# Kernel optimization log

Hardware: AMD Instinct MI355X
Metric: run time of the kernel (lower is better)

The kernel has to match this reference:

```python
import jax, jax.numpy as jnp
import numpy as np

N_NODES = 65536
IN_DIM = 512
OUT_DIM = 512
N_EDGES = 524288
BN_EPS = 1e-5
NORM_EPS = 1e-6


def setup_inputs() -> dict:
    key = jax.random.key(0)
    k1, k2, k3, k4 = jax.random.split(key, 4)
    features = jax.random.normal(k1, (N_NODES, IN_DIM), dtype=jnp.float32)
    edge_index = jax.random.randint(k2, (2, N_EDGES), 0, N_NODES, dtype=jnp.int64)
    # torch Linear weight layout: [out_features, in_features] with in = 2*IN_DIM
    W = jax.random.normal(k3, (OUT_DIM, 2 * IN_DIM), dtype=jnp.float32) * (1.0 / np.sqrt(2 * IN_DIM))
    b = jax.random.normal(k4, (OUT_DIM,), dtype=jnp.float32) * 0.01
    gamma = jnp.ones((OUT_DIM,), dtype=jnp.float32)
    beta = jnp.zeros((OUT_DIM,), dtype=jnp.float32)
    running_mean = jnp.zeros((OUT_DIM,), dtype=jnp.float32)
    running_var = jnp.ones((OUT_DIM,), dtype=jnp.float32)
    return {
        "features": features,
        "edge_index": edge_index,
        "W": W,
        "b": b,
        "gamma": gamma,
        "beta": beta,
        "running_mean": running_mean,
        "running_var": running_var,
    }


def reference(features, edge_index, W, b, gamma, beta, running_mean, running_var):
    sources = edge_index[0]
    targets = edge_index[1]
    # scatter-sum of neighbor (target) features into source rows  [N, D]
    aggregated = jax.ops.segment_sum(features[targets], sources, num_segments=N_NODES)
    out = jnp.concatenate([features, aggregated], axis=1)  # [N, 2D]
    out = out @ W.T + b  # [N, OUT_DIM]
    out = jax.nn.relu(out)
    # BatchNorm1d (eval mode, running stats)
    out = (out - running_mean) * jax.lax.rsqrt(running_var + BN_EPS) * gamma + beta
    # dropout is identity in inference
    out = out / (jnp.linalg.norm(out, axis=1, keepdims=True) + NORM_EPS)
    return out
```

## Files before the change

### kernel.cpp

```cpp
#include <hip/hip_runtime.h>
#include <hip/hip_bf16.h>

#define N_NODES 65536
#define DIM 512
#define N_EDGES 524288
#define BN_EPS 1e-5f
#define NORM_EPS 1e-6f

typedef __attribute__((ext_vector_type(8))) short short8;
typedef __attribute__((ext_vector_type(4))) float f32x4;

static __device__ __forceinline__ unsigned f2bf(float f) {
    union { float f; unsigned u; } c; c.f = f;
    unsigned u = c.u;
    return (u + 0x7fffu + ((u >> 16) & 1u)) >> 16;
}
static __device__ __forceinline__ float bf16lo(unsigned u) {
    union { unsigned u; float f; } c; c.u = u << 16; return c.f;
}
static __device__ __forceinline__ float bf16hi(unsigned u) {
    union { unsigned u; float f; } c; c.u = u & 0xffff0000u; return c.f;
}
static __device__ __forceinline__ uint4 pack8(float4 a, float4 b) {
    uint4 o;
    o.x = f2bf(a.x) | (f2bf(a.y) << 16);
    o.y = f2bf(a.z) | (f2bf(a.w) << 16);
    o.z = f2bf(b.x) | (f2bf(b.y) << 16);
    o.w = f2bf(b.z) | (f2bf(b.w) << 16);
    return o;
}

__global__ void convert_kernel(const float* __restrict__ src,
                               unsigned short* __restrict__ dst, int n8) {
    int i = blockIdx.x * blockDim.x + threadIdx.x;
    if (i < n8) {
        const float4* s = (const float4*)src + i * 2;
        float4 f0 = s[0], f1 = s[1];
        ((uint4*)dst)[i] = pack8(f0, f1);
    }
}

__global__ void hist_kernel(const int* __restrict__ src, int* __restrict__ counts) {
    int e = blockIdx.x * blockDim.x + threadIdx.x;
    if (e < N_EDGES) atomicAdd(&counts[src[e]], 1);
}

__global__ void scan_partial(const int* __restrict__ counts, int* __restrict__ partials) {
    __shared__ int ws[4];
    int t = threadIdx.x;
    int v = counts[blockIdx.x * 256 + t];
#pragma unroll
    for (int d = 1; d < 64; d <<= 1) v += __shfl_xor(v, d);
    if ((t & 63) == 0) ws[t >> 6] = v;
    __syncthreads();
    if (t == 0) partials[blockIdx.x] = ws[0] + ws[1] + ws[2] + ws[3];
}

__global__ void scan_base(int* __restrict__ partials) {
    __shared__ int lds[256];
    int t = threadIdx.x;
    int v = partials[t];
    lds[t] = v;
    __syncthreads();
    for (int d = 1; d < 256; d <<= 1) {
        int mine = lds[t];
        int add = (t >= d) ? lds[t - d] : 0;
        __syncthreads();
        lds[t] = mine + add;
        __syncthreads();
    }
    partials[t] = lds[t] - v;
}

__global__ void scan_final(const int* __restrict__ counts,
                           const int* __restrict__ partials,
                           int* __restrict__ offsets, int* __restrict__ cursor) {
    __shared__ int lds[256];
    int t = threadIdx.x, b = blockIdx.x;
    int v = counts[b * 256 + t];
    lds[t] = v;
    __syncthreads();
    for (int d = 1; d < 256; d <<= 1) {
        int mine = lds[t];
        int add = (t >= d) ? lds[t - d] : 0;
        __syncthreads();
        lds[t] = mine + add;
        __syncthreads();
    }
    int excl = lds[t] - v + partials[b];
    offsets[b * 256 + t] = excl;
    cursor[b * 256 + t] = excl;
    if (b == 255 && t == 255) offsets[N_NODES] = excl + v;
}

__global__ void scatter_kernel(const int* __restrict__ src, const int* __restrict__ tgt,
                               int* __restrict__ cursor, int* __restrict__ sortedT) {
    int e = blockIdx.x * blockDim.x + threadIdx.x;
    if (e < N_EDGES) {
        int s = src[e];
        int pos = atomicAdd(&cursor[s], 1);
        sortedT[pos] = tgt[e];
    }
}

static __device__ __forceinline__ void acc8(float* a, uint4 v) {
    a[0] += bf16lo(v.x); a[1] += bf16hi(v.x);
    a[2] += bf16lo(v.y); a[3] += bf16hi(v.y);
    a[4] += bf16lo(v.z); a[5] += bf16hi(v.z);
    a[6] += bf16lo(v.w); a[7] += bf16hi(v.w);
}

__global__ void aggregate_kernel(const unsigned short* __restrict__ Xb,
                                 const int* __restrict__ offsets,
                                 const int* __restrict__ sortedT,
                                 unsigned short* __restrict__ agg) {
    int wave = (blockIdx.x * blockDim.x + threadIdx.x) >> 6;
    int lane = threadIdx.x & 63;
    if (wave >= N_NODES) return;
    int beg = offsets[wave], end = offsets[wave + 1];
    float a[8] = {0.f, 0.f, 0.f, 0.f, 0.f, 0.f, 0.f, 0.f};
    float b[8] = {0.f, 0.f, 0.f, 0.f, 0.f, 0.f, 0.f, 0.f};
    const uint4* F = (const uint4*)Xb;
    int i = beg;
    for (; i + 4 <= end; i += 4) {
        int t0 = sortedT[i], t1 = sortedT[i + 1], t2 = sortedT[i + 2], t3 = sortedT[i + 3];
        uint4 v0 = F[t0 * 64 + lane];
        uint4 v1 = F[t1 * 64 + lane];
        uint4 v2 = F[t2 * 64 + lane];
        uint4 v3 = F[t3 * 64 + lane];
        acc8(a, v0); acc8(b, v1); acc8(a, v2); acc8(b, v3);
    }
    if (i + 2 <= end) {
        int t0 = sortedT[i], t1 = sortedT[i + 1];
        uint4 v0 = F[t0 * 64 + lane];
        uint4 v1 = F[t1 * 64 + lane];
        acc8(a, v0); acc8(b, v1);
        i += 2;
    }
    if (i < end) {
        int t0 = sortedT[i];
        uint4 v0 = F[t0 * 64 + lane];
        acc8(a, v0);
    }
#pragma unroll
    for (int k = 0; k < 8; ++k) a[k] += b[k];
    uint4 o;
    o.x = f2bf(a[0]) | (f2bf(a[1]) << 16);
    o.y = f2bf(a[2]) | (f2bf(a[3]) << 16);
    o.z = f2bf(a[4]) | (f2bf(a[5]) << 16);
    o.w = f2bf(a[6]) | (f2bf(a[7]) << 16);
    ((uint4*)agg)[wave * 64 + lane] = o;
}

__global__ __launch_bounds__(512, 2) void fused_gemm_norm_kernel(
        const unsigned short* __restrict__ Xb,
        const unsigned short* __restrict__ agg,
        const unsigned short* __restrict__ Wb,
        const float* __restrict__ bias,
        const float* __restrict__ gamma,
        const float* __restrict__ beta,
        const float* __restrict__ rmean,
        const float* __restrict__ rvar,
        float* __restrict__ out) {
    __shared__ uint4 Abuf[2][512];
    __shared__ uint4 Bbuf[2][4096];
    float (*ssm)[8] = reinterpret_cast<float (*)[8]>(&Abuf[0][0]);

    const int t = threadIdx.x;
    const int m0 = blockIdx.x * 64;
    const int w = t >> 6, L = t & 63;
    const int ml = L & 15, quad = L >> 4;
    const int wn = w * 64;

    auto stage = [&](int buf, int kt) {
        const unsigned short* Asrc = (kt < 8) ? (Xb + kt * 64) : (agg + (kt - 8) * 64);
        {
            int r = t >> 3, pp = t & 7;
            int p = pp ^ (r & 7);
            const unsigned short* ga = Asrc + (m0 + r) * 512 + p * 8;
            char* la = (char*)&Abuf[buf][t & 448];
            __builtin_amdgcn_global_load_lds(
                (const __attribute__((address_space(1))) unsigned int*)ga,
                (__attribute__((address_space(3))) unsigned int*)la, 16, 0, 0);
        }
#pragma unroll
        for (int j = 0; j < 8; ++j) {
            int c = j * 64 + L;
            int rl = c >> 3, pp = c & 7;
            int p = pp ^ (rl & 7);
            const unsigned short* gb = Wb + (wn + rl) * 1024 + kt * 64 + p * 8;
            char* lb = (char*)&Bbuf[buf][w * 512 + j * 64];
            __builtin_amdgcn_global_load_lds(
                (const __attribute__((address_space(1))) unsigned int*)gb,
                (__attribute__((address_space(3))) unsigned int*)lb, 16, 0, 0);
        }
    };

    f32x4 acc[4][4];
#pragma unroll
    for (int mi = 0; mi < 4; ++mi)
#pragma unroll
        for (int ni = 0; ni < 4; ++ni)
            acc[mi][ni] = (f32x4){0.f, 0.f, 0.f, 0.f};

    stage(0, 0);
    __syncthreads();

    int cur = 0;
    for (int kt = 0; kt < 16; ++kt) {
        if (kt < 15) stage(cur ^ 1, kt + 1);
#pragma unroll
        for (int kc = 0; kc < 2; ++kc) {
            int g = kc * 4 + quad;
            short8 a[4], b[4];
#pragma unroll
            for (int mi = 0; mi < 4; ++mi) {
                int ra = mi * 16 + ml;
                a[mi] = *(const short8*)&Abuf[cur][ra * 8 + (g ^ (ra & 7))];
                int rl = mi * 16 + ml;
                b[mi] = *(const short8*)&Bbuf[cur][w * 512 + rl * 8 + (g ^ (rl & 7))];
            }
#pragma unroll
            for (int mi = 0; mi < 4; ++mi)
#pragma unroll
                for (int ni = 0; ni < 4; ++ni)
                    acc[mi][ni] = __builtin_amdgcn_mfma_f32_16x16x32_bf16(
                        a[mi], b[ni], acc[mi][ni], 0, 0, 0);
        }
        __syncthreads();
        cur ^= 1;
    }

    float bi[4], sc[4], sh[4];
#pragma unroll
    for (int ni = 0; ni < 4; ++ni) {
        int col = wn + ni * 16 + ml;
        bi[ni] = bias[col];
        sc[ni] = gamma[col] * __frsqrt_rn(rvar[col] + BN_EPS);
        sh[ni] = beta[col] - rmean[col] * sc[ni];
    }
    float ss[4][4];
#pragma unroll
    for (int mi = 0; mi < 4; ++mi)
#pragma unroll
        for (int r = 0; r < 4; ++r)
            ss[mi][r] = 0.f;
#pragma unroll
    for (int mi = 0; mi < 4; ++mi)
#pragma unroll
        for (int ni = 0; ni < 4; ++ni)
#pragma unroll
            for (int r = 0; r < 4; ++r) {
                float v = fmaxf(acc[mi][ni][r] + bi[ni], 0.f) * sc[ni] + sh[ni];
                acc[mi][ni][r] = v;
                ss[mi][r] += v * v;
            }
#pragma unroll
    for (int mi = 0; mi < 4; ++mi)
#pragma unroll
        for (int r = 0; r < 4; ++r) {
#pragma unroll
            for (int d = 1; d < 16; d <<= 1)
                ss[mi][r] += __shfl_xor(ss[mi][r], d);
        }
    if (ml == 0) {
#pragma unroll
        for (int mi = 0; mi < 4; ++mi)
#pragma unroll
            for (int r = 0; r < 4; ++r)
                ssm[mi * 16 + quad * 4 + r][w] = ss[mi][r];
    }
    __syncthreads();
#pragma unroll
    for (int mi = 0; mi < 4; ++mi)
#pragma unroll
        for (int r = 0; r < 4; ++r) {
            int rl = mi * 16 + quad * 4 + r;
            const float4* sp = (const float4*)ssm[rl];
            float4 s0 = sp[0], s1 = sp[1];
            float tot = s0.x + s0.y + s0.z + s0.w + s1.x + s1.y + s1.z + s1.w;
            float inv = 1.f / (sqrtf(tot) + NORM_EPS);
            int m = m0 + rl;
#pragma unroll
            for (int ni = 0; ni < 4; ++ni)
                out[m * 512 + wn + ni * 16 + ml] = acc[mi][ni][r] * inv;
        }
}

extern "C" void kernel_launch(void* const* d_in, const int* in_sizes, int n_in,
                              void* d_out, int out_size, void* d_ws, size_t ws_size,
                              hipStream_t stream) {
    const float* features = (const float*)d_in[0];
    const int* edges      = (const int*)d_in[1];
    const float* W        = (const float*)d_in[2];
    const float* bias     = (const float*)d_in[3];
    const float* gamma    = (const float*)d_in[4];
    const float* beta     = (const float*)d_in[5];
    const float* rmean    = (const float*)d_in[6];
    const float* rvar     = (const float*)d_in[7];
    float* out = (float*)d_out;

    char* ws = (char*)d_ws;
    int* counts   = (int*)(ws);
    int* offsets  = (int*)(ws + 0x100000);
    int* cursor   = (int*)(ws + 0x200000);
    int* partials = (int*)(ws + 0x280000);
    int* sortedT  = (int*)(ws + 0x300000);
    unsigned short* Wb  = (unsigned short*)(ws + 0x500000);
    unsigned short* Xb  = (unsigned short*)(ws + 0x600000);
    unsigned short* agg = (unsigned short*)(ws + 0x4600000);

    const int* src = edges;
    const int* tgt = edges + N_EDGES;

    hipMemsetAsync(counts, 0, N_NODES * sizeof(int), stream);
    hist_kernel<<<N_EDGES / 256, 256, 0, stream>>>(src, counts);
    scan_partial<<<256, 256, 0, stream>>>(counts, partials);
    scan_base<<<1, 256, 0, stream>>>(partials);
    scan_final<<<256, 256, 0, stream>>>(counts, partials, offsets, cursor);
    scatter_kernel<<<N_EDGES / 256, 256, 0, stream>>>(src, tgt, cursor, sortedT);
    convert_kernel<<<(N_NODES * DIM / 8) / 256, 256, 0, stream>>>(features, Xb, N_NODES * DIM / 8);
    convert_kernel<<<(DIM * 2 * DIM / 8) / 256, 256, 0, stream>>>(W, Wb, DIM * 2 * DIM / 8);
    aggregate_kernel<<<N_NODES / 4, 256, 0, stream>>>(Xb, offsets, sortedT, agg);
    fused_gemm_norm_kernel<<<N_NODES / 64, 512, 0, stream>>>(
        Xb, agg, Wb, bias, gamma, beta, rmean, rvar, out);
}
```

Measured before the change: 495.0 us.

## Double GEMM row tile to 128 with 16 waves and finer-grained waitcnt sync

The fused GEMM+norm kernel now runs 1024-thread blocks covering 128 rows, arranged as a 2x8 wave grid, so each staged W tile is shared by twice as many rows and W reload traffic is halved. The per-wave B staging becomes a cooperative block-wide load, and the full __syncthreads pairs are replaced by explicit vmcnt/lgkmcnt waits plus raw s_barrier so the next stage's loads can stay in flight. The cost is larger LDS use per block and a launch_bounds of (1024,4) that may tighten register limits and cause spills. Fewer, larger blocks also reduce the number of blocks per CU.

```diff
diff --git a/kernel.cpp b/kernel.cpp
--- a/kernel.cpp
+++ b/kernel.cpp
@@ -152,7 +152,7 @@
     ((uint4*)agg)[wave * 64 + lane] = o;
 }
 
-__global__ __launch_bounds__(512, 2) void fused_gemm_norm_kernel(
+__global__ __launch_bounds__(1024, 4) void fused_gemm_norm_kernel(
         const unsigned short* __restrict__ Xb,
         const unsigned short* __restrict__ agg,
         const unsigned short* __restrict__ Wb,
@@ -162,15 +162,16 @@
         const float* __restrict__ rmean,
         const float* __restrict__ rvar,
         float* __restrict__ out) {
-    __shared__ uint4 Abuf[2][512];
+    __shared__ uint4 Abuf[2][1024];
     __shared__ uint4 Bbuf[2][4096];
     float (*ssm)[8] = reinterpret_cast<float (*)[8]>(&Abuf[0][0]);
 
     const int t = threadIdx.x;
-    const int m0 = blockIdx.x * 64;
+    const int m0 = blockIdx.x * 128;
     const int w = t >> 6, L = t & 63;
     const int ml = L & 15, quad = L >> 4;
-    const int wn = w * 64;
+    const int wm = (w >> 3) * 64;
+    const int wn = (w & 7) * 64;
 
     auto stage = [&](int buf, int kt) {
         const unsigned short* Asrc = (kt < 8) ? (Xb + kt * 64) : (agg + (kt - 8) * 64);
@@ -178,18 +179,18 @@
             int r = t >> 3, pp = t & 7;
             int p = pp ^ (r & 7);
             const unsigned short* ga = Asrc + (m0 + r) * 512 + p * 8;
-            char* la = (char*)&Abuf[buf][t & 448];
+            char* la = (char*)&Abuf[buf][t & 960];
             __builtin_amdgcn_global_load_lds(
                 (const __attribute__((address_space(1))) unsigned int*)ga,
                 (__attribute__((address_space(3))) unsigned int*)la, 16, 0, 0);
         }
 #pragma unroll
-        for (int j = 0; j < 8; ++j) {
-            int c = j * 64 + L;
-            int rl = c >> 3, pp = c & 7;
-            int p = pp ^ (rl & 7);
-            const unsigned short* gb = Wb + (wn + rl) * 1024 + kt * 64 + p * 8;
-            char* lb = (char*)&Bbuf[buf][w * 512 + j * 64];
+        for (int j = 0; j < 4; ++j) {
+            int c = j * 1024 + t;
+            int r = c >> 3, pp = c & 7;
+            int p = pp ^ (r & 7);
+            const unsigned short* gb = Wb + r * 1024 + kt * 64 + p * 8;
+            char* lb = (char*)&Bbuf[buf][j * 1024 + (t & 960)];
             __builtin_amdgcn_global_load_lds(
                 (const __attribute__((address_space(1))) unsigned int*)gb,
                 (__attribute__((address_space(3))) unsigned int*)lb, 16, 0, 0);
@@ -204,21 +205,26 @@
             acc[mi][ni] = (f32x4){0.f, 0.f, 0.f, 0.f};
 
     stage(0, 0);
-    __syncthreads();
 
     int cur = 0;
     for (int kt = 0; kt < 16; ++kt) {
-        if (kt < 15) stage(cur ^ 1, kt + 1);
+        if (kt < 15) {
+            stage(cur ^ 1, kt + 1);
+            asm volatile("s_waitcnt vmcnt(5)" ::: "memory");
+        } else {
+            asm volatile("s_waitcnt vmcnt(0)" ::: "memory");
+        }
+        __builtin_amdgcn_s_barrier();
 #pragma unroll
         for (int kc = 0; kc < 2; ++kc) {
             int g = kc * 4 + quad;
             short8 a[4], b[4];
 #pragma unroll
-            for (int mi = 0; mi < 4; ++mi) {
-                int ra = mi * 16 + ml;
-                a[mi] = *(const short8*)&Abuf[cur][ra * 8 + (g ^ (ra & 7))];
-                int rl = mi * 16 + ml;
-                b[mi] = *(const short8*)&Bbuf[cur][w * 512 + rl * 8 + (g ^ (rl & 7))];
+            for (int x = 0; x < 4; ++x) {
+                int ra = wm + x * 16 + ml;
+                a[x] = *(const short8*)&Abuf[cur][ra * 8 + (g ^ (ra & 7))];
+                int rb = wn + x * 16 + ml;
+                b[x] = *(const short8*)&Bbuf[cur][rb * 8 + (g ^ (rb & 7))];
             }
 #pragma unroll
             for (int mi = 0; mi < 4; ++mi)
@@ -227,7 +233,8 @@
                     acc[mi][ni] = __builtin_amdgcn_mfma_f32_16x16x32_bf16(
                         a[mi], b[ni], acc[mi][ni], 0, 0, 0);
         }
-        __syncthreads();
+        asm volatile("s_waitcnt lgkmcnt(0)" ::: "memory");
+        __builtin_amdgcn_s_barrier();
         cur ^= 1;
     }
 
@@ -268,14 +275,14 @@
         for (int mi = 0; mi < 4; ++mi)
 #pragma unroll
             for (int r = 0; r < 4; ++r)
-                ssm[mi * 16 + quad * 4 + r][w] = ss[mi][r];
+                ssm[wm + mi * 16 + quad * 4 + r][w & 7] = ss[mi][r];
     }
     __syncthreads();
 #pragma unroll
     for (int mi = 0; mi < 4; ++mi)
 #pragma unroll
         for (int r = 0; r < 4; ++r) {
-            int rl = mi * 16 + quad * 4 + r;
+            int rl = wm + mi * 16 + quad * 4 + r;
             const float4* sp = (const float4*)ssm[rl];
             float4 s0 = sp[0], s1 = sp[1];
             float tot = s0.x + s0.y + s0.z + s0.w + s1.x + s1.y + s1.z + s1.w;
@@ -322,6 +329,6 @@
     convert_kernel<<<(N_NODES * DIM / 8) / 256, 256, 0, stream>>>(features, Xb, N_NODES * DIM / 8);
     convert_kernel<<<(DIM * 2 * DIM / 8) / 256, 256, 0, stream>>>(W, Wb, DIM * 2 * DIM / 8);
     aggregate_kernel<<<N_NODES / 4, 256, 0, stream>>>(Xb, offsets, sortedT, agg);
-    fused_gemm_norm_kernel<<<N_NODES / 64, 512, 0, stream>>>(
+    fused_gemm_norm_kernel<<<N_NODES / 128, 1024, 0, stream>>>(
         Xb, agg, Wb, bias, gamma, beta, rmean, rvar, out);
 }
```

New measurement: 459.1 us. -7.2%, faster.
